# Performance work log

Measured on AMD Instinct MI355X. Metric: run time of the kernel, lower is better.

The kernel has to match this reference:

```python
import jax, jax.numpy as jnp
import numpy as np
from jax import lax


def get_grid(h, w):
    # normalized [-1,1] grid, channel 0 = x, channel 1 = y, shape [1,h,w,2]
    gx, gy = jnp.meshgrid(jnp.linspace(-1.0, 1.0, w), jnp.linspace(-1.0, 1.0, h))
    return jnp.stack([gx, gy], axis=-1)[None].astype(jnp.float32)


def gaussian_kernel(k, sigma=1.0):
    c = jnp.arange(k, dtype=jnp.float32) - (k - 1) / 2.0
    g = jnp.exp(-(c ** 2) / (2.0 * sigma ** 2))
    k2 = jnp.outer(g, g)
    return k2 / k2.sum()


def resize_bilinear(x, H, W):
    # x: [B,C,h,w]; torch F.interpolate(mode='bilinear', align_corners=False)
    B, C, h, w = x.shape
    def coords(n_out, n_in):
        c = (jnp.arange(n_out, dtype=jnp.float32) + 0.5) * (n_in / n_out) - 0.5
        c = jnp.clip(c, 0.0, n_in - 1.0)
        lo = jnp.floor(c).astype(jnp.int32)
        hi = jnp.minimum(lo + 1, n_in - 1)
        return lo, hi, c - lo.astype(jnp.float32)
    y0, y1, wy = coords(H, h)
    x0, x1, wx = coords(W, w)
    r = x[:, :, y0, :] * (1.0 - wy)[None, None, :, None] + x[:, :, y1, :] * wy[None, None, :, None]
    return r[:, :, :, x0] * (1.0 - wx) + r[:, :, :, x1] * wx


def _forward(src_grid, kernel, src_grid_base, tgt_grid, niter):
    B = src_grid.shape[0]
    H, W = tgt_grid.shape[1], tgt_grid.shape[2]
    ks = kernel.shape[-1]
    HW = H * W
    # forward displacement, resampled to target resolution, in pixel units
    dsrc = (src_grid - src_grid_base).transpose(0, 3, 1, 2)        # [B,2,Hs,Ws]
    dsrc = resize_bilinear(dsrc, H, W)                              # [B,2,H,W]
    dx = dsrc[:, 0].reshape(B, HW) * (W / 2.0)
    dy = dsrc[:, 1].reshape(B, HW) * (H / 2.0)
    xg = (jnp.arange(HW) % W).astype(jnp.float32)
    yg = (jnp.arange(HW) // W).astype(jnp.float32)
    xi = jnp.round(xg[None] + dx).astype(jnp.int32)
    yi = jnp.round(yg[None] + dy).astype(jnp.int32)
    oob = (xi < 0) | (yi < 0) | (xi > W - 1) | (yi > H - 1)
    field = jnp.where(oob, -1, yi * W + xi) + 1   # index 0 = trash slot
    # sort + dedup: duplicates are redirected to the trash slot
    order = jnp.argsort(field, axis=1)            # stable
    sf = jnp.take_along_axis(field, order, axis=1)
    keep = jnp.concatenate([jnp.ones((B, 1), bool), sf[:, 1:] != sf[:, :-1]], axis=1)
    sf = sf * keep
    inv_order = jnp.argsort(order, axis=1)
    field = jnp.take_along_axis(sf, inv_order, axis=1)
    # scatter inverse displacement (unique indices except trash slot 0)
    z = jnp.zeros((B, 1), dtype=dx.dtype)
    dxp = jnp.concatenate([z, dx], axis=1)
    dyp = jnp.concatenate([z, dy], axis=1)
    fieldp = jnp.concatenate([jnp.zeros((B, 1), field.dtype), field], axis=1)
    bidx = jnp.arange(B)[:, None]
    inv_dx = jnp.zeros_like(dxp).at[bidx, fieldp].set(-dxp)[:, 1:].reshape(B, H, W)
    inv_dy = jnp.zeros_like(dyp).at[bidx, fieldp].set(-dyp)[:, 1:].reshape(B, H, W)
    mask = (jnp.zeros_like(dxp).at[bidx, fieldp].set(1.0)[:, 1:].reshape(B, H, W)) > 0.5
    # pad so hole-fill never reads outside
    p = niter + 1
    inv_dx = jnp.pad(inv_dx, ((0, 0), (p, p), (p, p)))
    inv_dy = jnp.pad(inv_dy, ((0, 0), (p, p), (p, p)))
    mask = jnp.pad(mask, ((0, 0), (p, p), (p, p)))
    pd = ks // 2
    k4 = kernel.reshape(1, 1, ks, ks)
    def conv(x):
        return lax.conv_general_dilated(x[:, None], k4, (1, 1), [(pd, pd), (pd, pd)])[:, 0]
    # hole-fill: dilate mask by 4-neighborhood, fill with gaussian-weighted avg
    for _ in range(niter):
        nb = (jnp.pad(mask, ((0, 0), (1, 0), (0, 0)))[:, :-1]
              | jnp.pad(mask, ((0, 0), (0, 1), (0, 0)))[:, 1:]
              | jnp.pad(mask, ((0, 0), (0, 0), (1, 0)))[:, :, :-1]
              | jnp.pad(mask, ((0, 0), (0, 0), (0, 1)))[:, :, 1:])
        new_mask = (~mask) & nb
        new_dx = conv(inv_dx)
        new_dy = conv(inv_dy)
        new_sum = conv(mask.astype(inv_dx.dtype))
        denom = jnp.where(new_mask, new_sum, 1.0)  # safe: new_sum>0 where new_mask
        inv_dx = jnp.where(new_mask, new_dx / denom, inv_dx)
        inv_dy = jnp.where(new_mask, new_dy / denom, inv_dy)
        mask = mask | new_mask
    # erode: drop pixels with any unmasked 4-neighbor (outside counts as masked)
    for _ in range(niter):
        full = (jnp.pad(mask, ((0, 0), (1, 0), (0, 0)), constant_values=True)[:, :-1]
                & jnp.pad(mask, ((0, 0), (0, 1), (0, 0)), constant_values=True)[:, 1:]
                & jnp.pad(mask, ((0, 0), (0, 0), (1, 0)), constant_values=True)[:, :, :-1]
                & jnp.pad(mask, ((0, 0), (0, 0), (0, 1)), constant_values=True)[:, :, 1:])
        mask = mask & full
    inv_dx = jnp.where(mask, inv_dx, 2.0 * W)
    inv_dy = jnp.where(mask, inv_dy, 2.0 * H)
    inv_dx = inv_dx[:, p:-p, p:-p]
    inv_dy = inv_dy[:, p:-p, p:-p]
    dtgt = jnp.stack([inv_dx * (2.0 / W), inv_dy * (2.0 / H)], axis=3)
    return tgt_grid + dtgt


def setup_inputs() -> dict:
    key = jax.random.key(0)
    B, Hs, Ws, H, W = 8, 256, 256, 512, 512
    base = get_grid(Hs, Ws)
    src_grid = base + 0.05 * jax.random.normal(key, (B, Hs, Ws, 2), jnp.float32)
    return {
        "src_grid": src_grid,
        "kernel": gaussian_kernel(3),
        "src_grid_base": base,
        "tgt_grid": get_grid(H, W),
        "niter": 5,
    }


def reference(src_grid, kernel, src_grid_base, tgt_grid, niter):
    return _forward(src_grid, kernel, src_grid_base, tgt_grid, niter)
```

## Files before the change

kernel.cpp:

```cpp
#include <hip/hip_runtime.h>
#include <hip/hip_fp16.h>

typedef unsigned long long u64;
typedef unsigned int u32;
typedef float float4a __attribute__((ext_vector_type(4), aligned(4)));

#define B_    8
#define HS_   256
#define WS_   256
#define H_    512
#define W_    512
#define HW_   (H_ * W_)
#define TO_Y  8
#define NTY   64
#define BND   16
#define NB    32
#define WR    28
#define COFF  6
#define PC    524
#define VSTR  531
#define INFW  0xFFFFFFFFu
#define CAPB  16384

__device__ __forceinline__ void bilin_disp(const float* __restrict__ src,
                                           const float* __restrict__ base,
                                           int b, int y, int x,
                                           float& dx, float& dy) {
#pragma clang fp contract(off)
    float cy = ((float)y + 0.5f) * 0.5f - 0.5f;
    cy = fminf(fmaxf(cy, 0.0f), 255.0f);
    int   y0 = (int)floorf(cy);
    int   y1 = min(y0 + 1, HS_ - 1);
    float wy = cy - (float)y0;

    float cx = ((float)x + 0.5f) * 0.5f - 0.5f;
    cx = fminf(fmaxf(cx, 0.0f), 255.0f);
    int   x0 = (int)floorf(cx);
    float wx = cx - (float)x0;

    float omy = 1.0f - wy;
    float wA, wB;
    int xs;
    if (x0 >= WS_ - 1) { xs = WS_ - 2; wA = 0.0f; wB = 1.0f; }
    else               { xs = x0;      wA = 1.0f - wx; wB = wx; }

    const float4a* S0 = (const float4a*)(src  + ((b * HS_ + y0) * WS_ + xs) * 2);
    const float4a* S1 = (const float4a*)(src  + ((b * HS_ + y1) * WS_ + xs) * 2);
    const float4a* B0 = (const float4a*)(base + (y0 * WS_ + xs) * 2);
    const float4a* B1 = (const float4a*)(base + (y1 * WS_ + xs) * 2);
    float4a s0 = *S0, s1 = *S1, b0 = *B0, b1 = *B1;

    float a00x = s0.x - b0.x, a00y = s0.y - b0.y;
    float a01x = s0.z - b0.z, a01y = s0.w - b0.w;
    float a10x = s1.x - b1.x, a10y = s1.y - b1.y;
    float a11x = s1.z - b1.z, a11y = s1.w - b1.w;

    float r0x = a00x * omy + a10x * wy;
    float r0y = a00y * omy + a10y * wy;
    float r1x = a01x * omy + a11x * wy;
    float r1y = a01y * omy + a11y * wy;
    dx = (r0x * wA + r1x * wB) * 256.0f;
    dy = (r0y * wA + r1y * wB) * 256.0f;
}

__device__ __forceinline__ u32 pack16(float x, float y) {
    __half hx = __float2half_rn(x), hy = __float2half_rn(y);
    return ((u32)__half_as_ushort(hy) << 16) | (u32)__half_as_ushort(hx);
}
__device__ __forceinline__ float2 unpack16(u32 p) {
    float2 f;
    f.x = __half2float(__ushort_as_half((unsigned short)(p & 0xFFFFu)));
    f.y = __half2float(__ushort_as_half((unsigned short)(p >> 16)));
    return f;
}

__device__ __forceinline__ u64 shfl_left(u64 v) {
    unsigned lo = __shfl_up((unsigned)v, 1);
    unsigned hi = __shfl_up((unsigned)(v >> 32), 1);
    u64 r = ((u64)hi << 32) | lo;
    return (threadIdx.x & 63) ? r : 0ull;
}
__device__ __forceinline__ u64 shfl_right(u64 v) {
    unsigned lo = __shfl_down((unsigned)v, 1);
    unsigned hi = __shfl_down((unsigned)(v >> 32), 1);
    u64 r = ((u64)hi << 32) | lo;
    return ((threadIdx.x & 63) == 63) ? 0ull : r;
}

__launch_bounds__(1024)
__global__ void pre_k(const float* __restrict__ src,
                      const float* __restrict__ base,
                      u32* __restrict__ pay,
                      u32* __restrict__ gcount,
                      u32* __restrict__ bucket) {
    __shared__ u32 cnt[NB];
    __shared__ u32 bbase[NB];

    int bid = blockIdx.x;
    int b   = bid & 7;
    int t   = bid >> 3;
    int j   = t * 1024 + threadIdx.x;
    int y   = j >> 9;
    int x   = j & (W_ - 1);

    if (threadIdx.x < NB) cnt[threadIdx.x] = 0;
    __syncthreads();

    float dx, dy;
    bilin_disp(src, base, b, y, x, dx, dy);
    pay[b * HW_ + j] = pack16(-dx, -dy);

    int xi = (int)rintf((float)x + dx);
    int yi = (int)rintf((float)y + dy);
    bool inb = (xi >= 0 && xi < W_ && yi >= 0 && yi < H_);
    int band = 0, rank = 0;
    if (inb) {
        band = yi >> 4;
        rank = atomicAdd(&cnt[band], 1u);
    }
    __syncthreads();
    if (threadIdx.x < NB && cnt[threadIdx.x] > 0)
        bbase[threadIdx.x] = atomicAdd(&gcount[b * NB + threadIdx.x],
                                       cnt[threadIdx.x]);
    __syncthreads();
    if (inb) {
        u32 slotn = bbase[band] + rank;
        if (slotn < CAPB) {
            u32 e = ((u32)(yi & 15) << 27) | ((u32)xi << 18) | (u32)j;
            bucket[(b * NB + band) * CAPB + slotn] = e;
        }
    }
}

__launch_bounds__(1024, 8)
__global__ void fused4_k(const u32* __restrict__ pay,
                         const u32* __restrict__ gcount,
                         const u32* __restrict__ bucket,
                         const float* __restrict__ kern,
                         const float* __restrict__ tgt,
                         float* __restrict__ out) {
    __shared__ u32 plane[WR * VSTR];

    int id   = blockIdx.x;
    int b    = id & 7;
    int tile = id >> 3;
    int Y0   = tile * TO_Y;
    int w0   = Y0 - 10;
    int tid  = threadIdx.x;

    float kw[9];
#pragma unroll
    for (int q = 0; q < 9; q++) kw[q] = kern[q];

    for (int i = tid; i < WR * VSTR; i += 1024) plane[i] = INFW;
    __syncthreads();

    {
        int qlo = max(0, w0 >> 4);
        int qhi = min(NB - 1, (w0 + WR - 1) >> 4);
        for (int q = qlo; q <= qhi; q++) {
            u32 cntq = min(gcount[b * NB + q], (u32)CAPB);
            const u32* bk = bucket + (b * NB + q) * CAPB;
            int ybase = q * BND - w0;
            for (u32 i = tid; i < cntq; i += 1024) {
                u32 e  = bk[i];
                int wr = ybase + (int)((e >> 27) & 15u);
                if ((unsigned)wr < WR) {
                    int xc = (int)((e >> 18) & 511u);
                    atomicMin(&plane[wr * VSTR + xc + COFF], e & 0x3FFFFu);
                }
            }
        }
    }
    __syncthreads();

    int wv   = tid >> 6;
    int lane = tid & 63;
    int col  = 32 * wv - 16 + lane;
    int cls  = col + COFF;
    bool colin = (col >= -COFF) && (col <= W_ + 5);

    u64 m = 0;
    if (colin) {
#pragma unroll 7
        for (int r = 0; r < WR; r++)
            m |= (u64)(plane[r * VSTR + cls] != INFW) << r;
    }
    __syncthreads();

    {
        const u32* pb = pay + b * HW_;
        for (int idx = tid; idx < WR * PC; idx += 1024) {
            int rr = idx / PC;
            int cc = idx - rr * PC;
            int off = rr * VSTR + cc;
            u32 k = plane[off];
            plane[off] = (k != INFW) ? pb[k] : 0u;
        }
    }
    __syncthreads();

    int rlo = max(0, -COFF - w0);
    int rhi = min(WR - 1, (W_ + 5) - w0);
    u64 validm = colin ? ((((u64)1 << (rhi - rlo + 1)) - 1) << rlo) : 0ull;

    const u64 VROWS = (((u64)1 << 16) - 1) << 6;
    bool vlane = (lane >= 6 && lane <= 57);

    for (int it = 0; it < 5; it++) {
        u64 mL = shfl_left(m), mR = shfl_right(m);
        u64 cand = ~m & ((m << 1) | (m >> 1) | mL | mR) & validm;
        u64 cv = vlane ? (cand & VROWS) : 0ull;
        while (cv) {
            int r = __builtin_ctzll(cv);
            cv &= cv - 1;
            float s = 0.0f, ax = 0.0f, ay = 0.0f;
#pragma unroll
            for (int dr = -1; dr <= 1; dr++) {
#pragma unroll
                for (int dc = -1; dc <= 1; dc++) {
                    if (dr == 0 && dc == 0) continue;
                    u64 nm = (dc < 0) ? mL : ((dc > 0) ? mR : m);
                    float wq = ((nm >> (r + dr)) & 1)
                                 ? kw[(dr + 1) * 3 + (dc + 1)] : 0.0f;
                    int cc = min(max(cls + dc, 0), PC - 1);
                    float2 nv = unpack16(plane[(r + dr) * VSTR + cc]);
                    s += wq; ax += wq * nv.x; ay += wq * nv.y;
                }
            }
            float rs = __builtin_amdgcn_rcpf(s);
            plane[r * VSTR + cls] = pack16(ax * rs, ay * rs);
        }
        m |= cand;
        __syncthreads();
    }

    for (int it = 0; it < 5; it++) {
        u64 mL = shfl_left(m), mR = shfl_right(m);
        m &= (m << 1) & (m >> 1) & mL & mR;
    }

    if (lane >= 16 && lane < 48) {
#pragma unroll 4
        for (int r = 10; r < 10 + TO_Y; r++) {
            int row = w0 + r;
            bool on = (m >> r) & 1;
            float vx, vy;
            if (on) {
                float2 t = unpack16(plane[r * VSTR + cls]);
                vx = t.x * (1.0f / 256.0f);
                vy = t.y * (1.0f / 256.0f);
            } else {
                vx = 4.0f; vy = 4.0f;
            }
            int ti = (row * W_ + col) * 2;
            float2 tg = *(const float2*)(tgt + ti);
            float2 ov; ov.x = tg.x + vx; ov.y = tg.y + vy;
            ((float2*)out)[(size_t)b * HW_ + row * W_ + col] = ov;
        }
    }
}

extern "C" void kernel_launch(void* const* d_in, const int* in_sizes, int n_in,
                              void* d_out, int out_size, void* d_ws, size_t ws_size,
                              hipStream_t stream) {
    const float* src  = (const float*)d_in[0];
    const float* kern = (const float*)d_in[1];
    const float* base = (const float*)d_in[2];
    const float* tgt  = (const float*)d_in[3];
    float* out = (float*)d_out;

    char* ws = (char*)d_ws;
    u32* gcount = (u32*)ws;
    u32* pay    = (u32*)(ws + 1024);
    u32* bucket = (u32*)(ws + 1024 + (size_t)B_ * HW_ * 4);

    hipMemsetAsync(gcount, 0, B_ * NB * sizeof(u32), stream);

    pre_k<<<(B_ * HW_) / 1024, 1024, 0, stream>>>(src, base, pay, gcount, bucket);
    fused4_k<<<512, 1024, 0, stream>>>(pay, gcount, bucket, kern, tgt, out);
}
```

Before: 139.7 us.

## Split fused kernel into half-width tiles with taller rows and column buckets

The scatter buckets are now split by row band and by image half, and entries near the middle column are written to both halves. Each fused block now covers a 16-row by 256-column tile with 512 threads instead of an 8-row full-width tile with 1024 threads. The halo overhead per output row shrinks (36 window rows for 16 output rows instead of 28 for 8), so less scatter, gather and smoothing work is spent on halo. In exchange, halo columns are duplicated, each bucket holds half as many entries (CAPB is 8192), and each thread handles more rows in the smoothing loop.

```diff
diff --git a/kernel.cpp b/kernel.cpp
--- a/kernel.cpp
+++ b/kernel.cpp
@@ -11,16 +11,15 @@
 #define H_    512
 #define W_    512
 #define HW_   (H_ * W_)
-#define TO_Y  8
-#define NTY   64
-#define BND   16
-#define NB    32
-#define WR    28
-#define COFF  6
-#define PC    524
-#define VSTR  531
+#define TO_Y  16
+#define NTILE 32
+#define WR    36
+#define WCOLS 276
+#define WSTR  277
+#define NBAND 32
+#define NBKT  64
 #define INFW  0xFFFFFFFFu
-#define CAPB  16384
+#define CAPB  8192
 
 __device__ __forceinline__ void bilin_disp(const float* __restrict__ src,
                                            const float* __restrict__ base,
@@ -93,8 +92,8 @@
                       u32* __restrict__ pay,
                       u32* __restrict__ gcount,
                       u32* __restrict__ bucket) {
-    __shared__ u32 cnt[NB];
-    __shared__ u32 bbase[NB];
+    __shared__ u32 cnt[NBKT];
+    __shared__ u32 bbase[NBKT];
 
     int bid = blockIdx.x;
     int b   = bid & 7;
@@ -103,7 +102,7 @@
     int y   = j >> 9;
     int x   = j & (W_ - 1);
 
-    if (threadIdx.x < NB) cnt[threadIdx.x] = 0;
+    if (threadIdx.x < NBKT) cnt[threadIdx.x] = 0;
     __syncthreads();
 
     float dx, dy;
@@ -113,61 +112,75 @@
     int xi = (int)rintf((float)x + dx);
     int yi = (int)rintf((float)y + dy);
     bool inb = (xi >= 0 && xi < W_ && yi >= 0 && yi < H_);
-    int band = 0, rank = 0;
+    int bk0 = 0, bk1 = -1;
+    u32 r0 = 0, r1 = 0, e = 0;
     if (inb) {
-        band = yi >> 4;
-        rank = atomicAdd(&cnt[band], 1u);
-    }
-    __syncthreads();
-    if (threadIdx.x < NB && cnt[threadIdx.x] > 0)
-        bbase[threadIdx.x] = atomicAdd(&gcount[b * NB + threadIdx.x],
-                                       cnt[threadIdx.x]);
+        int band = yi >> 4;
+        bk0 = band * 2 + (xi >> 8);
+        r0 = atomicAdd(&cnt[bk0], 1u);
+        if      (xi >= 246 && xi <= 255) bk1 = band * 2 + 1;
+        else if (xi >= 256 && xi <= 265) bk1 = band * 2;
+        if (bk1 >= 0) r1 = atomicAdd(&cnt[bk1], 1u);
+        e = ((u32)(yi & 15) << 27) | ((u32)xi << 18) | (u32)j;
+    }
+    __syncthreads();
+    if (threadIdx.x < NBKT) {
+        u32 c = cnt[threadIdx.x];
+        bbase[threadIdx.x] = c ? atomicAdd(&gcount[b * NBKT + threadIdx.x], c)
+                               : 0u;
+    }
     __syncthreads();
     if (inb) {
-        u32 slotn = bbase[band] + rank;
-        if (slotn < CAPB) {
-            u32 e = ((u32)(yi & 15) << 27) | ((u32)xi << 18) | (u32)j;
-            bucket[(b * NB + band) * CAPB + slotn] = e;
-        }
-    }
-}
-
-__launch_bounds__(1024, 8)
-__global__ void fused4_k(const u32* __restrict__ pay,
+        u32 s0 = bbase[bk0] + r0;
+        if (s0 < CAPB) bucket[(b * NBKT + bk0) * CAPB + s0] = e;
+        if (bk1 >= 0) {
+            u32 s1 = bbase[bk1] + r1;
+            if (s1 < CAPB) bucket[(b * NBKT + bk1) * CAPB + s1] = e;
+        }
+    }
+}
+
+__launch_bounds__(512, 2)
+__global__ void fused5_k(const u32* __restrict__ pay,
                          const u32* __restrict__ gcount,
                          const u32* __restrict__ bucket,
                          const float* __restrict__ kern,
                          const float* __restrict__ tgt,
                          float* __restrict__ out) {
-    __shared__ u32 plane[WR * VSTR];
+    __shared__ u32 plane[WR * WSTR];
 
     int id   = blockIdx.x;
     int b    = id & 7;
-    int tile = id >> 3;
+    int rest = id >> 3;
+    int tile = rest >> 1;
+    int half = rest & 1;
+    int X0   = half << 8;
     int Y0   = tile * TO_Y;
     int w0   = Y0 - 10;
+    int wc0  = X0 - 10;
     int tid  = threadIdx.x;
 
     float kw[9];
 #pragma unroll
     for (int q = 0; q < 9; q++) kw[q] = kern[q];
 
-    for (int i = tid; i < WR * VSTR; i += 1024) plane[i] = INFW;
+    for (int i = tid; i < WR * WSTR; i += 512) plane[i] = INFW;
     __syncthreads();
 
     {
         int qlo = max(0, w0 >> 4);
-        int qhi = min(NB - 1, (w0 + WR - 1) >> 4);
+        int qhi = min(NBAND - 1, (w0 + WR - 1) >> 4);
         for (int q = qlo; q <= qhi; q++) {
-            u32 cntq = min(gcount[b * NB + q], (u32)CAPB);
-            const u32* bk = bucket + (b * NB + q) * CAPB;
-            int ybase = q * BND - w0;
-            for (u32 i = tid; i < cntq; i += 1024) {
+            int bki = b * NBKT + q * 2 + half;
+            u32 cntq = min(gcount[bki], (u32)CAPB);
+            const u32* bk = bucket + bki * CAPB;
+            int ybase = q * 16 - w0;
+            for (u32 i = tid; i < cntq; i += 512) {
                 u32 e  = bk[i];
                 int wr = ybase + (int)((e >> 27) & 15u);
                 if ((unsigned)wr < WR) {
-                    int xc = (int)((e >> 18) & 511u);
-                    atomicMin(&plane[wr * VSTR + xc + COFF], e & 0x3FFFFu);
+                    int xc = (int)((e >> 18) & 511u) - wc0;
+                    atomicMin(&plane[wr * WSTR + xc], e & 0x3FFFFu);
                 }
             }
         }
@@ -176,35 +189,36 @@
 
     int wv   = tid >> 6;
     int lane = tid & 63;
-    int col  = 32 * wv - 16 + lane;
-    int cls  = col + COFF;
-    bool colin = (col >= -COFF) && (col <= W_ + 5);
+    int col  = X0 + 32 * wv - 16 + lane;
+    int cls  = col - wc0;
+    bool inwin = ((unsigned)cls < WCOLS);
+    bool colin = inwin && (col >= -6) && (col <= W_ + 5);
 
     u64 m = 0;
     if (colin) {
-#pragma unroll 7
+#pragma unroll 6
         for (int r = 0; r < WR; r++)
-            m |= (u64)(plane[r * VSTR + cls] != INFW) << r;
+            m |= (u64)(plane[r * WSTR + cls] != INFW) << r;
     }
     __syncthreads();
 
     {
         const u32* pb = pay + b * HW_;
-        for (int idx = tid; idx < WR * PC; idx += 1024) {
-            int rr = idx / PC;
-            int cc = idx - rr * PC;
-            int off = rr * VSTR + cc;
+        for (int idx = tid; idx < WR * WCOLS; idx += 512) {
+            int rr = idx / WCOLS;
+            int cc = idx - rr * WCOLS;
+            int off = rr * WSTR + cc;
             u32 k = plane[off];
             plane[off] = (k != INFW) ? pb[k] : 0u;
         }
     }
     __syncthreads();
 
-    int rlo = max(0, -COFF - w0);
+    int rlo = max(0, -6 - w0);
     int rhi = min(WR - 1, (W_ + 5) - w0);
     u64 validm = colin ? ((((u64)1 << (rhi - rlo + 1)) - 1) << rlo) : 0ull;
 
-    const u64 VROWS = (((u64)1 << 16) - 1) << 6;
+    const u64 VROWS = (((u64)1 << 24) - 1) << 6;
     bool vlane = (lane >= 6 && lane <= 57);
 
     for (int it = 0; it < 5; it++) {
@@ -223,13 +237,13 @@
                     u64 nm = (dc < 0) ? mL : ((dc > 0) ? mR : m);
                     float wq = ((nm >> (r + dr)) & 1)
                                  ? kw[(dr + 1) * 3 + (dc + 1)] : 0.0f;
-                    int cc = min(max(cls + dc, 0), PC - 1);
-                    float2 nv = unpack16(plane[(r + dr) * VSTR + cc]);
+                    int cc = min(max(cls + dc, 0), WCOLS - 1);
+                    float2 nv = unpack16(plane[(r + dr) * WSTR + cc]);
                     s += wq; ax += wq * nv.x; ay += wq * nv.y;
                 }
             }
             float rs = __builtin_amdgcn_rcpf(s);
-            plane[r * VSTR + cls] = pack16(ax * rs, ay * rs);
+            plane[r * WSTR + cls] = pack16(ax * rs, ay * rs);
         }
         m |= cand;
         __syncthreads();
@@ -247,7 +261,7 @@
             bool on = (m >> r) & 1;
             float vx, vy;
             if (on) {
-                float2 t = unpack16(plane[r * VSTR + cls]);
+                float2 t = unpack16(plane[r * WSTR + cls]);
                 vx = t.x * (1.0f / 256.0f);
                 vy = t.y * (1.0f / 256.0f);
             } else {
@@ -272,11 +286,11 @@
 
     char* ws = (char*)d_ws;
     u32* gcount = (u32*)ws;
-    u32* pay    = (u32*)(ws + 1024);
-    u32* bucket = (u32*)(ws + 1024 + (size_t)B_ * HW_ * 4);
-
-    hipMemsetAsync(gcount, 0, B_ * NB * sizeof(u32), stream);
+    u32* pay    = (u32*)(ws + 4096);
+    u32* bucket = (u32*)(ws + 4096 + (size_t)B_ * HW_ * 4);
+
+    hipMemsetAsync(gcount, 0, B_ * NBKT * sizeof(u32), stream);
 
     pre_k<<<(B_ * HW_) / 1024, 1024, 0, stream>>>(src, base, pay, gcount, bucket);
-    fused4_k<<<512, 1024, 0, stream>>>(pay, gcount, bucket, kern, tgt, out);
-}
+    fused5_k<<<512, 512, 0, stream>>>(pay, gcount, bucket, kern, tgt, out);
+}
```

New measurement: 136.9 us. 2.0% less time.
